# Optimization experiments

Measured on AMD Instinct MI355X. Metric: run time of the kernel, lower is better.

Reference implementation:

```python
import jax, jax.numpy as jnp
import numpy as np

B, T, H, V, L = 16, 256, 512, 32, 2


def setup_inputs() -> dict:
    key = jax.random.key(0)
    ks = jax.random.split(key, 24)
    s = 1.0 / np.sqrt(H)
    d = {}
    d["encoder_outputs"] = jax.random.normal(ks[0], (B, T, H), jnp.float32)
    d["h0"] = jax.random.normal(ks[1], (L, B, H), jnp.float32)
    d["c0"] = jax.random.normal(ks[2], (L, B, H), jnp.float32)
    d["audio_lengths"] = jax.random.randint(ks[3], (B,), 1, T + 1, jnp.int32)
    d["Wq"] = jax.random.normal(ks[4], (H, H), jnp.float32) * s
    d["bq"] = jnp.zeros((H,), jnp.float32)
    d["Wk"] = jax.random.normal(ks[5], (H, H), jnp.float32) * s
    d["bk"] = jnp.zeros((H,), jnp.float32)
    d["v"] = jax.random.normal(ks[6], (H,), jnp.float32) * s
    d["vb"] = jnp.zeros((1,), jnp.float32)
    d["Wih0"] = jax.random.normal(ks[7], (4 * H, 2 * H), jnp.float32) * s
    d["bih0"] = jnp.zeros((4 * H,), jnp.float32)
    d["Whh0"] = jax.random.normal(ks[8], (4 * H, H), jnp.float32) * s
    d["bhh0"] = jnp.zeros((4 * H,), jnp.float32)
    d["Wih1"] = jax.random.normal(ks[9], (4 * H, H), jnp.float32) * s
    d["bih1"] = jnp.zeros((4 * H,), jnp.float32)
    d["Whh1"] = jax.random.normal(ks[10], (4 * H, H), jnp.float32) * s
    d["bhh1"] = jnp.zeros((4 * H,), jnp.float32)
    d["Wout"] = jax.random.normal(ks[11], (V, H), jnp.float32) * s
    d["bout"] = jnp.zeros((V,), jnp.float32)
    return d


def _lstm_cell(x, h, c, Wih, bih, Whh, bhh):
    # PyTorch gate order: i, f, g, o
    g = x @ Wih.T + bih + h @ Whh.T + bhh
    i, f, gg, o = jnp.split(g, 4, axis=-1)
    c2 = jax.nn.sigmoid(f) * c + jax.nn.sigmoid(i) * jnp.tanh(gg)
    h2 = jax.nn.sigmoid(o) * jnp.tanh(c2)
    return h2, c2


def reference(encoder_outputs, h0, c0, audio_lengths, Wq, bq, Wk, bk, v, vb,
              Wih0, bih0, Whh0, bhh0, Wih1, bih1, Whh1, bhh1, Wout, bout):
    # Precompute key projection once (same math as per-step Wk @ keys)
    Kproj = encoder_outputs @ Wk.T + bk  # [B,T,H]

    def step(carry, enc_t):
        h, c = carry  # each [L,B,H]
        q = h[-1]  # [B,H] top-layer hidden drives attention
        e = jnp.tanh((q @ Wq.T + bq)[:, None, :] + Kproj)  # [B,T,H]
        scores = jnp.einsum('bth,h->bt', e, v) + vb[0]  # [B,T]
        w = jax.nn.softmax(scores, axis=-1)
        ctx = jnp.einsum('bt,bth->bh', w, encoder_outputs)  # [B,H]
        x = jnp.concatenate([enc_t, ctx], axis=-1)  # [B,2H]
        h0n, c0n = _lstm_cell(x, h[0], c[0], Wih0, bih0, Whh0, bhh0)
        h1n, c1n = _lstm_cell(h0n, h[1], c[1], Wih1, bih1, Whh1, bhh1)
        logit = h1n @ Wout.T + bout  # [B,V]
        return (jnp.stack([h0n, h1n]), jnp.stack([c0n, c1n])), logit

    _, logits = jax.lax.scan(step, (h0, c0), jnp.swapaxes(encoder_outputs, 0, 1))
    return jnp.swapaxes(logits, 0, 1)  # [B,T,V]
```

## Files before the change

kernel.cpp:

```cpp
#include <hip/hip_runtime.h>

#define HH 512
#define BB 16
#define TT 256
#define VV 32
#define TPB 256
#define NBLK 256
#define PITCH 516

#define BAR_INTS 512

struct KArgs {
  const float* enc; const float* h0in; const float* c0in;
  const float* Wq; const float* bq; const float* vatt; const float* vb;
  const float* Wih0; const float* bih0; const float* Whh0; const float* bhh0;
  const float* Wih1; const float* bih1; const float* Whh1; const float* bhh1;
  const float* Wout; const float* bout;
  const float* Kproj; float* H0buf; float* H1buf; float* qWg; float* Ug; float* Zg;
  int* bar; float* out;
};

struct Smem {
  float W0e[4][2][PITCH];
  float W0c[4][2][PITCH];
  float W0h[4][2][PITCH];
  float W1x[4][2][PITCH];
  float W1h[4][2][PITCH];
  float Wqr[2][PITCH];
  float Wor[2][PITCH];
  float vv[HH];
  float qrow[HH];
  float stg[BB][PITCH];
  float red[4][64];
  float pre0[BB][4][2];
  float pre1[BB][4][2];
  float cst[2][2][BB];
  float scw[16];
  float zinv[BB];
  float bs0[4][2];
  float bs1[4][2];
  float bqv[2], boutv[2];
};

__device__ __forceinline__ float fsig(float x){ return 1.0f/(1.0f + __expf(-x)); }
__device__ __forceinline__ float ftanh(float x){
  float ee = __expf(2.0f*x);
  return 1.0f - 2.0f/(ee + 1.0f);
}

__device__ __forceinline__ void stcc(float* p, float v){
  __hip_atomic_store(p, v, __ATOMIC_RELAXED, __HIP_MEMORY_SCOPE_AGENT);
}
__device__ __forceinline__ float ldcc(const float* p){
  return __hip_atomic_load(p, __ATOMIC_RELAXED, __HIP_MEMORY_SCOPE_AGENT);
}
__device__ __forceinline__ float2 ld2cc(const float* p){
  unsigned long long v = __hip_atomic_load((const unsigned long long*)p,
                                           __ATOMIC_RELAXED, __HIP_MEMORY_SCOPE_AGENT);
  union { unsigned long long u; float2 f; } c; c.u = v;
  return c.f;
}

__device__ __forceinline__ void ldbuf_cc(const float* __restrict__ src,
                                         float2* __restrict__ v, int tid){
  #pragma unroll
  for (int it = 0; it < 16; ++it)
    v[it] = ld2cc(&src[(it*TPB + tid)*2]);
}
__device__ __forceinline__ void stg_regs(const float2* __restrict__ v,
                                         float (* __restrict__ stg)[PITCH], int tid){
  #pragma unroll
  for (int it = 0; it < 16; ++it){
    const int i2 = (it*TPB + tid)*2;
    *(float2*)&stg[i2 >> 9][i2 & 511] = v[it];
  }
}

__device__ __forceinline__ void gbar_arrive(int* __restrict__ bar, int e, int bid){
  __syncthreads();
  if (threadIdx.x == 0)
    __hip_atomic_store(&bar[bid], e, __ATOMIC_RELAXED, __HIP_MEMORY_SCOPE_AGENT);
}
__device__ __forceinline__ void gbar_wait(int* __restrict__ bar, int e, int bid){
  if (threadIdx.x < 64){
    const unsigned long long* p = (const unsigned long long*)bar;
    const int i0 = threadIdx.x * 2;
    int spins = 0;
    for (;;){
      unsigned long long v0 = __hip_atomic_load(&p[i0],     __ATOMIC_RELAXED, __HIP_MEMORY_SCOPE_AGENT);
      unsigned long long v1 = __hip_atomic_load(&p[i0 + 1], __ATOMIC_RELAXED, __HIP_MEMORY_SCOPE_AGENT);
      const int a0 = (int)v0, a1 = (int)(v0 >> 32), a2 = (int)v1, a3 = (int)(v1 >> 32);
      const int ok = (a0 >= e) & (a1 >= e) & (a2 >= e) & (a3 >= e);
      if (__all(ok)) break;
      __builtin_amdgcn_s_sleep(2);
      if (++spins > (1 << 20)) break;
    }
  }
  __syncthreads();
}
__device__ __forceinline__ void gbar(int* __restrict__ bar, int e, int bid){
  gbar_arrive(bar, e, bid);
  gbar_wait(bar, e, bid);
}

__device__ __forceinline__ void gbar2(int* __restrict__ bar2, int et, int bid, int ba){
  __syncthreads();
  if (threadIdx.x == 0)
    __hip_atomic_store(&bar2[bid], et, __ATOMIC_RELAXED, __HIP_MEMORY_SCOPE_AGENT);
  if (threadIdx.x < 64){
    const unsigned long long* p = (const unsigned long long*)bar2 + ba*8;
    int spins = 0;
    for (;;){
      int ok = 1;
      if (threadIdx.x < 8){
        unsigned long long v = __hip_atomic_load(&p[threadIdx.x], __ATOMIC_RELAXED, __HIP_MEMORY_SCOPE_AGENT);
        ok = ((int)v >= et) & ((int)(v >> 32) >= et);
      }
      if (__all(ok)) break;
      __builtin_amdgcn_s_sleep(1);
      if (++spins > (1 << 20)) break;
    }
  }
  __syncthreads();
}

__device__ __forceinline__ void dot_part(const float* __restrict__ W,
                                         const float (* __restrict__ stg)[PITCH],
                                         float (* __restrict__ red)[64],
                                         int wave, int lane){
  const int jj = wave >> 1, off = (wave & 1) << 8;
  const int b = lane & 15, g = lane >> 4;
  const float* wrow = W + (size_t)(g*2 + jj)*PITCH + off;
  const float* xrow = &stg[b][off];
  float acc = 0.f;
  #pragma unroll 8
  for (int h = 0; h < 256; h += 4){
    const float4 w4 = *(const float4*)&wrow[h];
    const float4 x4 = *(const float4*)&xrow[h];
    acc = fmaf(w4.x,x4.x, fmaf(w4.y,x4.y, fmaf(w4.z,x4.z, fmaf(w4.w,x4.w, acc))));
  }
  red[wave][lane] = acc;
}

__global__ void init_kernel(const float* __restrict__ h0in, float* __restrict__ H0buf,
                            float* __restrict__ H1buf, float* __restrict__ Ug,
                            float* __restrict__ Zg, int* __restrict__ bar){
  const int i = blockIdx.x*blockDim.x + threadIdx.x;
  if (i < BB*HH){
    H0buf[i] = h0in[i];
    H1buf[i] = h0in[BB*HH + i];
  }
  if (i < 2*BB*HH) Ug[i] = 0.0f;
  if (i < 32) Zg[i] = 0.0f;
  if (i < BAR_INTS) bar[i] = 0;
}

__global__ __launch_bounds__(256, 1) void kproj_kernel(const float* __restrict__ enc,
                                                       const float* __restrict__ Wk,
                                                       const float* __restrict__ bk,
                                                       float* __restrict__ Kproj){
  __shared__ float er[BB][PITCH];
  const int bid = blockIdx.x, tid = threadIdx.x;
  const int wave = tid >> 6, lane = tid & 63;
  const int r = lane & 15, q = lane >> 4;
  const int row0 = bid*16;
  #pragma unroll
  for (int it = 0; it < 8; ++it){
    const int idx = (it*256 + tid)*4;
    const int rr = idx >> 9, h = idx & 511;
    *(float4*)&er[rr][h] = *(const float4*)&enc[(size_t)(row0+rr)*HH + h];
  }
  __syncthreads();
  float4 xr[32];
  #pragma unroll
  for (int i = 0; i < 32; ++i) xr[i] = *(const float4*)&er[r][q*128 + i*4];
  for (int k = 0; k < 128; ++k){
    const int hk = wave*128 + k;
    const float* wrow = Wk + (size_t)hk*HH + q*128;
    float acc = 0.f;
    #pragma unroll
    for (int i = 0; i < 32; ++i){
      const float4 w4 = *(const float4*)&wrow[i*4];
      acc = fmaf(w4.x,xr[i].x, fmaf(w4.y,xr[i].y, fmaf(w4.z,xr[i].z, fmaf(w4.w,xr[i].w, acc))));
    }
    acc += __shfl_xor(acc, 16);
    acc += __shfl_xor(acc, 32);
    if (lane < 16) Kproj[(size_t)(row0 + r)*HH + hk] = acc + bk[hk];
  }
}

__global__ __launch_bounds__(TPB, 1) void decoder_persist(KArgs a){
  __shared__ Smem S;
  const int bid = blockIdx.x, tid = threadIdx.x;
  const int wave = tid >> 6, lane = tid & 63;
  const int lb = lane & 15, lg = lane >> 4;
  const int j0 = bid*2;
  const int ba = bid >> 4, tb = (bid & 15) * 16;
  int* bar2 = a.bar + 256;

  for (int g = 0; g < 4; ++g){
    for (int jj = 0; jj < 2; ++jj){
      const int row = g*HH + j0 + jj;
      for (int h = tid; h < HH; h += TPB){
        S.W0e[g][jj][h] = a.Wih0[(size_t)row*(2*HH) + h];
        S.W0c[g][jj][h] = a.Wih0[(size_t)row*(2*HH) + HH + h];
        S.W0h[g][jj][h] = a.Whh0[(size_t)row*HH + h];
        S.W1x[g][jj][h] = a.Wih1[(size_t)row*HH + h];
        S.W1h[g][jj][h] = a.Whh1[(size_t)row*HH + h];
      }
    }
  }
  for (int jj = 0; jj < 2; ++jj){
    const int d = bid*2 + jj, vo = d & 31;
    for (int h = tid; h < HH; h += TPB){
      S.Wqr[jj][h] = a.Wq[(size_t)(j0+jj)*HH + h];
      S.Wor[jj][h] = a.Wout[(size_t)vo*HH + h];
    }
  }
  for (int h = tid; h < HH; h += TPB) S.vv[h] = a.vatt[h];
  if (tid < 16){
    S.cst[0][0][tid] = a.c0in[0*BB*HH + tid*HH + j0];
    S.cst[0][1][tid] = a.c0in[0*BB*HH + tid*HH + j0 + 1];
    S.cst[1][0][tid] = a.c0in[1*BB*HH + tid*HH + j0];
    S.cst[1][1][tid] = a.c0in[1*BB*HH + tid*HH + j0 + 1];
  }
  if (tid < 8){
    const int g = tid & 3, jj = tid >> 2;
    const int row = g*HH + j0 + jj;
    S.bs0[g][jj] = a.bih0[row] + a.bhh0[row];
    S.bs1[g][jj] = a.bih1[row] + a.bhh1[row];
  }
  if (tid < 2){
    S.bqv[tid] = a.bq[j0 + tid];
    S.boutv[tid] = a.bout[(bid*2 + tid) & 31];
  }
  const float vb0 = a.vb[0];

  float r_kp[4][8];
  #pragma unroll
  for (int i = 0; i < 4; ++i){
    const float* kp = a.Kproj + (size_t)(ba*TT + tb + wave*4 + i)*HH;
    #pragma unroll
    for (int k = 0; k < 8; ++k) r_kp[i][k] = kp[lane + 64*k];
  }
  float r_e0[16], r_e1[16];
  #pragma unroll
  for (int lt = 0; lt < 16; ++lt){
    const float* er = a.enc + (size_t)(ba*TT + tb + lt)*HH;
    r_e0[lt] = er[tid];
    r_e1[lt] = er[tid + 256];
  }
  float4 r_en[8];
  #pragma unroll
  for (int it = 0; it < 8; ++it){
    const int idx = (it*TPB + tid)*4;
    r_en[it] = *(const float4*)&a.enc[(size_t)((idx >> 9)*TT + 0)*HH + (idx & 511)];
  }
  __syncthreads();

  {
    #pragma unroll
    for (int it = 0; it < 8; ++it){
      const int idx = (it*TPB + tid)*4;
      *(float4*)&S.stg[idx >> 9][idx & 511] = *(const float4*)&a.h0in[idx];
    }
    __syncthreads();
    dot_part(&S.W0h[0][0][0], S.stg, S.red, wave, lane);
    __syncthreads();
    if (tid < 128){
      const int jj = tid >> 6, l = tid & 63, g = l >> 4, b = l & 15;
      S.pre0[b][g][jj] = S.red[2*jj][l] + S.red[2*jj+1][l] + S.bs0[g][jj];
    }
    __syncthreads();
  }

  int e = 0;
  for (int t = 0; t < TT; ++t){
    const int par = t & 1, parn = par ^ 1;

    float2 r_h1[16];
    ldbuf_cc(a.H1buf + par*(BB*HH), r_h1, tid);
    stg_regs(r_h1, S.stg, tid);
    __syncthreads();

    if (wave < 2){
      if (t > 0){
        const int d = bid*2 + wave, bo = d >> 5, vo = d & 31;
        float acc = 0.f;
        #pragma unroll
        for (int k = 0; k < 8; ++k){
          const int h = lane + 64*k;
          acc = fmaf(S.Wor[wave][h], S.stg[bo][h], acc);
        }
        #pragma unroll
        for (int off = 32; off; off >>= 1) acc += __shfl_xor(acc, off);
        if (lane == 0) a.out[(size_t)(bo*TT + (t-1))*VV + vo] = acc + S.boutv[wave];
      }
    } else {
      const int jj = wave - 2;
      const int off0 = lg * 128;
      float acc = 0.f;
      #pragma unroll 8
      for (int h = 0; h < 128; h += 4){
        const float4 w4 = *(const float4*)&S.Wqr[jj][off0 + h];
        const float4 x4 = *(const float4*)&S.stg[lb][off0 + h];
        acc = fmaf(w4.x,x4.x, fmaf(w4.y,x4.y, fmaf(w4.z,x4.z, fmaf(w4.w,x4.w, acc))));
      }
      acc += __shfl_xor(acc, 16);
      acc += __shfl_xor(acc, 32);
      if (lane < 16) stcc(&a.qWg[lane*HH + j0 + jj], acc + S.bqv[jj]);
    }

    e++; gbar_arrive(a.bar, e, bid);

    dot_part(&S.W1h[0][0][0], S.stg, S.red, wave, lane);
    __syncthreads();
    if (tid < 128){
      const int jj = tid >> 6, l = tid & 63, g = l >> 4, b = l & 15;
      S.pre1[b][g][jj] = S.red[2*jj][l] + S.red[2*jj+1][l] + S.bs1[g][jj];
    }
    #pragma unroll
    for (int it = 0; it < 8; ++it){
      const int idx = (it*TPB + tid)*4;
      *(float4*)&S.stg[idx >> 9][idx & 511] = r_en[it];
    }
    __syncthreads();
    dot_part(&S.W0e[0][0][0], S.stg, S.red, wave, lane);
    __syncthreads();
    if (tid < 128){
      const int jj = tid >> 6, l = tid & 63, g = l >> 4, b = l & 15;
      S.pre0[b][g][jj] += S.red[2*jj][l] + S.red[2*jj+1][l];
    }

    gbar_wait(a.bar, e, bid);

    {
      float* Up = a.Ug + par*(BB*HH);
      float* Zp = a.Zg + par*16;
      const float2 q2 = ld2cc(&a.qWg[ba*HH + tid*2]);
      *(float2*)&S.qrow[tid*2] = q2;
      __syncthreads();
      #pragma unroll
      for (int i = 0; i < 4; ++i){
        float acc = 0.f;
        #pragma unroll
        for (int k = 0; k < 8; ++k){
          const int h = lane + 64*k;
          acc = fmaf(S.vv[h], ftanh(S.qrow[h] + r_kp[i][k]), acc);
        }
        #pragma unroll
        for (int off = 32; off; off >>= 1) acc += __shfl_xor(acc, off);
        if (lane == 0) S.scw[wave*4 + i] = __expf(acc + vb0);
      }
      __syncthreads();
      float u0 = 0.f, u1 = 0.f;
      #pragma unroll
      for (int lt = 0; lt < 16; ++lt){
        const float w = S.scw[lt];
        u0 = fmaf(w, r_e0[lt], u0);
        u1 = fmaf(w, r_e1[lt], u1);
      }
      unsafeAtomicAdd(&Up[ba*HH + tid],       u0);
      unsafeAtomicAdd(&Up[ba*HH + tid + 256], u1);
      if (tid == 0){
        float zs = 0.f;
        #pragma unroll
        for (int lt = 0; lt < 16; ++lt) zs += S.scw[lt];
        unsafeAtomicAdd(&Zp[ba], zs);
      }
    }
    gbar2(bar2, t + 1, bid, ba);

    {
      float2 r_u[16];
      ldbuf_cc(a.Ug + par*(BB*HH), r_u, tid);
      if (tid < 16) S.zinv[tid] = 1.0f / ldcc(&a.Zg[par*16 + tid]);
      stg_regs(r_u, S.stg, tid);
      __syncthreads();
      dot_part(&S.W0c[0][0][0], S.stg, S.red, wave, lane);
      __syncthreads();
      if (tid < 32){
        const int b = tid & 15, jj = tid >> 4;
        const float zi = S.zinv[b];
        float gv[4];
        #pragma unroll
        for (int g = 0; g < 4; ++g)
          gv[g] = S.pre0[b][g][jj] + (S.red[2*jj][g*16+b] + S.red[2*jj+1][g*16+b]) * zi;
        const float cold = S.cst[0][jj][b];
        const float ii = fsig(gv[0]), ff = fsig(gv[1]);
        const float gg = ftanh(gv[2]), oo = fsig(gv[3]);
        const float cn = ff*cold + ii*gg;
        S.cst[0][jj][b] = cn;
        stcc(&a.H0buf[parn*(BB*HH) + b*HH + j0 + jj], oo * ftanh(cn));
      }
    }
    e++; gbar_arrive(a.bar, e, bid);
    {
      const int tn = (t + 1 < TT) ? (t + 1) : t;
      #pragma unroll
      for (int it = 0; it < 8; ++it){
        const int idx = (it*TPB + tid)*4;
        r_en[it] = *(const float4*)&a.enc[(size_t)((idx >> 9)*TT + tn)*HH + (idx & 511)];
      }
    }
    gbar_wait(a.bar, e, bid);

    {
      if (tid < 32) stcc(&a.Ug[parn*(BB*HH) + bid*32 + tid], 0.0f);
      if (bid == 0 && tid < 16) stcc(&a.Zg[parn*16 + tid], 0.0f);

      float2 r_x[16];
      ldbuf_cc(a.H0buf + parn*(BB*HH), r_x, tid);
      stg_regs(r_x, S.stg, tid);
      __syncthreads();
      dot_part(&S.W1x[0][0][0], S.stg, S.red, wave, lane);
      __syncthreads();
      if (tid < 32){
        const int b = tid & 15, jj = tid >> 4;
        float gv[4];
        #pragma unroll
        for (int g = 0; g < 4; ++g)
          gv[g] = S.pre1[b][g][jj] + S.red[2*jj][g*16+b] + S.red[2*jj+1][g*16+b];
        const float cold = S.cst[1][jj][b];
        const float ii = fsig(gv[0]), ff = fsig(gv[1]);
        const float gg = ftanh(gv[2]), oo = fsig(gv[3]);
        const float cn = ff*cold + ii*gg;
        S.cst[1][jj][b] = cn;
        stcc(&a.H1buf[parn*(BB*HH) + b*HH + j0 + jj], oo * ftanh(cn));
      }
    }
    e++; gbar_arrive(a.bar, e, bid);
    {
      dot_part(&S.W0h[0][0][0], S.stg, S.red, wave, lane);
      __syncthreads();
      if (tid < 128){
        const int jj = tid >> 6, l = tid & 63, g = l >> 4, b = l & 15;
        S.pre0[b][g][jj] = S.red[2*jj][l] + S.red[2*jj+1][l] + S.bs0[g][jj];
      }
    }
    gbar_wait(a.bar, e, bid);
  }

  {
    float2 r_x[16];
    ldbuf_cc(a.H1buf, r_x, tid);
    stg_regs(r_x, S.stg, tid);
    __syncthreads();
    if (wave < 2){
      const int d = bid*2 + wave, bo = d >> 5, vo = d & 31;
      float acc = 0.f;
      #pragma unroll
      for (int k = 0; k < 8; ++k){
        const int h = lane + 64*k;
        acc = fmaf(S.Wor[wave][h], S.stg[bo][h], acc);
      }
      #pragma unroll
      for (int off = 32; off; off >>= 1) acc += __shfl_xor(acc, off);
      if (lane == 0) a.out[(size_t)(bo*TT + 255)*VV + vo] = acc + S.boutv[wave];
    }
  }
}

extern "C" void kernel_launch(void* const* d_in, const int* in_sizes, int n_in,
                              void* d_out, int out_size, void* d_ws, size_t ws_size,
                              hipStream_t stream){
  const float* enc  = (const float*)d_in[0];
  const float* h0in = (const float*)d_in[1];
  const float* c0in = (const float*)d_in[2];
  const float* Wq   = (const float*)d_in[4];
  const float* bq   = (const float*)d_in[5];
  const float* Wk   = (const float*)d_in[6];
  const float* bk   = (const float*)d_in[7];
  const float* vatt = (const float*)d_in[8];
  const float* vb   = (const float*)d_in[9];
  const float* Wih0 = (const float*)d_in[10];
  const float* bih0 = (const float*)d_in[11];
  const float* Whh0 = (const float*)d_in[12];
  const float* bhh0 = (const float*)d_in[13];
  const float* Wih1 = (const float*)d_in[14];
  const float* bih1 = (const float*)d_in[15];
  const float* Whh1 = (const float*)d_in[16];
  const float* bhh1 = (const float*)d_in[17];
  const float* Wout = (const float*)d_in[18];
  const float* bout = (const float*)d_in[19];

  float* ws    = (float*)d_ws;
  float* Kproj = ws;
  float* H0buf = Kproj + (size_t)BB*TT*HH;
  float* H1buf = H0buf + 2*BB*HH;
  float* qWg   = H1buf + 2*BB*HH;
  float* Ug    = qWg + BB*HH;
  float* Zg    = Ug + 2*BB*HH;
  int*   bar   = (int*)(Zg + 32);

  hipLaunchKernelGGL(init_kernel, dim3(64), dim3(256), 0, stream,
                     h0in, H0buf, H1buf, Ug, Zg, bar);
  hipLaunchKernelGGL(kproj_kernel, dim3(256), dim3(256), 0, stream, enc, Wk, bk, Kproj);

  KArgs ka;
  ka.enc = enc; ka.h0in = h0in; ka.c0in = c0in;
  ka.Wq = Wq; ka.bq = bq; ka.vatt = vatt; ka.vb = vb;
  ka.Wih0 = Wih0; ka.bih0 = bih0; ka.Whh0 = Whh0; ka.bhh0 = bhh0;
  ka.Wih1 = Wih1; ka.bih1 = bih1; ka.Whh1 = Whh1; ka.bhh1 = bhh1;
  ka.Wout = Wout; ka.bout = bout;
  ka.Kproj = Kproj; ka.H0buf = H0buf; ka.H1buf = H1buf;
  ka.qWg = qWg; ka.Ug = Ug; ka.Zg = Zg; ka.bar = bar; ka.out = (float*)d_out;

  void* params[] = { (void*)&ka };
  hipLaunchCooperativeKernel((const void*)decoder_persist, dim3(NBLK), dim3(TPB),
                             params, 0, stream);
}
```

Measured before the change: 5.321 ms.

## Double threads per block to 512 and split dot products across eight waves

Raises the persistent kernel's block size from 256 to 512 threads, so every per-step gate matvec is split over eight waves with a four-way partial reduction instead of two-way. Per-thread register arrays, the attention key-projection tiles and the encoder context accumulation are halved to match. The reduction scratch is unioned with the query row to save LDS, and the inner loops use multiple accumulators for more ILP. Each latency-bound recurrent step is meant to finish sooner, at the cost of more intra-block synchronisation and a larger final reduction.

```diff
diff --git a/kernel.cpp b/kernel.cpp
--- a/kernel.cpp
+++ b/kernel.cpp
@@ -4,7 +4,7 @@
 #define BB 16
 #define TT 256
 #define VV 32
-#define TPB 256
+#define TPB 512
 #define NBLK 256
 #define PITCH 516
 
@@ -29,9 +29,8 @@
   float Wqr[2][PITCH];
   float Wor[2][PITCH];
   float vv[HH];
-  float qrow[HH];
+  union { float qrow[HH]; float red[8][64]; } qr;
   float stg[BB][PITCH];
-  float red[4][64];
   float pre0[BB][4][2];
   float pre1[BB][4][2];
   float cst[2][2][BB];
@@ -64,13 +63,13 @@
 __device__ __forceinline__ void ldbuf_cc(const float* __restrict__ src,
                                          float2* __restrict__ v, int tid){
   #pragma unroll
-  for (int it = 0; it < 16; ++it)
+  for (int it = 0; it < 8; ++it)
     v[it] = ld2cc(&src[(it*TPB + tid)*2]);
 }
 __device__ __forceinline__ void stg_regs(const float2* __restrict__ v,
                                          float (* __restrict__ stg)[PITCH], int tid){
   #pragma unroll
-  for (int it = 0; it < 16; ++it){
+  for (int it = 0; it < 8; ++it){
     const int i2 = (it*TPB + tid)*2;
     *(float2*)&stg[i2 >> 9][i2 & 511] = v[it];
   }
@@ -98,10 +97,6 @@
   }
   __syncthreads();
 }
-__device__ __forceinline__ void gbar(int* __restrict__ bar, int e, int bid){
-  gbar_arrive(bar, e, bid);
-  gbar_wait(bar, e, bid);
-}
 
 __device__ __forceinline__ void gbar2(int* __restrict__ bar2, int et, int bid, int ba){
   __syncthreads();
@@ -124,22 +119,27 @@
   __syncthreads();
 }
 
-__device__ __forceinline__ void dot_part(const float* __restrict__ W,
-                                         const float (* __restrict__ stg)[PITCH],
-                                         float (* __restrict__ red)[64],
-                                         int wave, int lane){
-  const int jj = wave >> 1, off = (wave & 1) << 8;
+__device__ __forceinline__ void dot8(const float* __restrict__ W,
+                                     const float (* __restrict__ stg)[PITCH],
+                                     float (* __restrict__ red)[64],
+                                     int wave, int lane){
+  const int jj = wave >> 2, off = (wave & 3) << 7;
   const int b = lane & 15, g = lane >> 4;
   const float* wrow = W + (size_t)(g*2 + jj)*PITCH + off;
   const float* xrow = &stg[b][off];
-  float acc = 0.f;
-  #pragma unroll 8
-  for (int h = 0; h < 256; h += 4){
-    const float4 w4 = *(const float4*)&wrow[h];
-    const float4 x4 = *(const float4*)&xrow[h];
-    acc = fmaf(w4.x,x4.x, fmaf(w4.y,x4.y, fmaf(w4.z,x4.z, fmaf(w4.w,x4.w, acc))));
-  }
-  red[wave][lane] = acc;
+  float a0 = 0.f, a1 = 0.f, a2 = 0.f, a3 = 0.f;
+  #pragma unroll
+  for (int h = 0; h < 128; h += 16){
+    const float4 w0 = *(const float4*)&wrow[h];      const float4 x0 = *(const float4*)&xrow[h];
+    const float4 w1 = *(const float4*)&wrow[h + 4];  const float4 x1 = *(const float4*)&xrow[h + 4];
+    const float4 w2 = *(const float4*)&wrow[h + 8];  const float4 x2 = *(const float4*)&xrow[h + 8];
+    const float4 w3 = *(const float4*)&wrow[h + 12]; const float4 x3 = *(const float4*)&xrow[h + 12];
+    a0 = fmaf(w0.x,x0.x, fmaf(w0.y,x0.y, fmaf(w0.z,x0.z, fmaf(w0.w,x0.w, a0))));
+    a1 = fmaf(w1.x,x1.x, fmaf(w1.y,x1.y, fmaf(w1.z,x1.z, fmaf(w1.w,x1.w, a1))));
+    a2 = fmaf(w2.x,x2.x, fmaf(w2.y,x2.y, fmaf(w2.z,x2.z, fmaf(w2.w,x2.w, a2))));
+    a3 = fmaf(w3.x,x3.x, fmaf(w3.y,x3.y, fmaf(w3.z,x3.z, fmaf(w3.w,x3.w, a3))));
+  }
+  red[wave][lane] = (a0 + a1) + (a2 + a3);
 }
 
 __global__ void init_kernel(const float* __restrict__ h0in, float* __restrict__ H0buf,
@@ -236,23 +236,20 @@
   }
   const float vb0 = a.vb[0];
 
-  float r_kp[4][8];
-  #pragma unroll
-  for (int i = 0; i < 4; ++i){
-    const float* kp = a.Kproj + (size_t)(ba*TT + tb + wave*4 + i)*HH;
+  float r_kp[2][8];
+  #pragma unroll
+  for (int i = 0; i < 2; ++i){
+    const float* kp = a.Kproj + (size_t)(ba*TT + tb + wave*2 + i)*HH;
     #pragma unroll
     for (int k = 0; k < 8; ++k) r_kp[i][k] = kp[lane + 64*k];
   }
-  float r_e0[16], r_e1[16];
-  #pragma unroll
-  for (int lt = 0; lt < 16; ++lt){
-    const float* er = a.enc + (size_t)(ba*TT + tb + lt)*HH;
-    r_e0[lt] = er[tid];
-    r_e1[lt] = er[tid + 256];
-  }
-  float4 r_en[8];
-  #pragma unroll
-  for (int it = 0; it < 8; ++it){
+  float r_e[16];
+  #pragma unroll
+  for (int lt = 0; lt < 16; ++lt)
+    r_e[lt] = a.enc[(size_t)(ba*TT + tb + lt)*HH + tid];
+  float4 r_en[4];
+  #pragma unroll
+  for (int it = 0; it < 4; ++it){
     const int idx = (it*TPB + tid)*4;
     r_en[it] = *(const float4*)&a.enc[(size_t)((idx >> 9)*TT + 0)*HH + (idx & 511)];
   }
@@ -260,16 +257,17 @@
 
   {
     #pragma unroll
-    for (int it = 0; it < 8; ++it){
+    for (int it = 0; it < 4; ++it){
       const int idx = (it*TPB + tid)*4;
       *(float4*)&S.stg[idx >> 9][idx & 511] = *(const float4*)&a.h0in[idx];
     }
     __syncthreads();
-    dot_part(&S.W0h[0][0][0], S.stg, S.red, wave, lane);
+    dot8(&S.W0h[0][0][0], S.stg, S.qr.red, wave, lane);
     __syncthreads();
     if (tid < 128){
       const int jj = tid >> 6, l = tid & 63, g = l >> 4, b = l & 15;
-      S.pre0[b][g][jj] = S.red[2*jj][l] + S.red[2*jj+1][l] + S.bs0[g][jj];
+      S.pre0[b][g][jj] = (S.qr.red[jj*4+0][l] + S.qr.red[jj*4+1][l])
+                       + (S.qr.red[jj*4+2][l] + S.qr.red[jj*4+3][l]) + S.bs0[g][jj];
     }
     __syncthreads();
   }
@@ -278,7 +276,7 @@
   for (int t = 0; t < TT; ++t){
     const int par = t & 1, parn = par ^ 1;
 
-    float2 r_h1[16];
+    float2 r_h1[8];
     ldbuf_cc(a.H1buf + par*(BB*HH), r_h1, tid);
     stg_regs(r_h1, S.stg, tid);
     __syncthreads();
@@ -296,16 +294,20 @@
         for (int off = 32; off; off >>= 1) acc += __shfl_xor(acc, off);
         if (lane == 0) a.out[(size_t)(bo*TT + (t-1))*VV + vo] = acc + S.boutv[wave];
       }
-    } else {
+    } else if (wave < 4){
       const int jj = wave - 2;
       const int off0 = lg * 128;
-      float acc = 0.f;
-      #pragma unroll 8
-      for (int h = 0; h < 128; h += 4){
-        const float4 w4 = *(const float4*)&S.Wqr[jj][off0 + h];
-        const float4 x4 = *(const float4*)&S.stg[lb][off0 + h];
-        acc = fmaf(w4.x,x4.x, fmaf(w4.y,x4.y, fmaf(w4.z,x4.z, fmaf(w4.w,x4.w, acc))));
-      }
+      float a0 = 0.f, a1 = 0.f;
+      #pragma unroll
+      for (int h = 0; h < 128; h += 8){
+        const float4 w0 = *(const float4*)&S.Wqr[jj][off0 + h];
+        const float4 x0 = *(const float4*)&S.stg[lb][off0 + h];
+        const float4 w1 = *(const float4*)&S.Wqr[jj][off0 + h + 4];
+        const float4 x1 = *(const float4*)&S.stg[lb][off0 + h + 4];
+        a0 = fmaf(w0.x,x0.x, fmaf(w0.y,x0.y, fmaf(w0.z,x0.z, fmaf(w0.w,x0.w, a0))));
+        a1 = fmaf(w1.x,x1.x, fmaf(w1.y,x1.y, fmaf(w1.z,x1.z, fmaf(w1.w,x1.w, a1))));
+      }
+      float acc = a0 + a1;
       acc += __shfl_xor(acc, 16);
       acc += __shfl_xor(acc, 32);
       if (lane < 16) stcc(&a.qWg[lane*HH + j0 + jj], acc + S.bqv[jj]);
@@ -313,23 +315,25 @@
 
     e++; gbar_arrive(a.bar, e, bid);
 
-    dot_part(&S.W1h[0][0][0], S.stg, S.red, wave, lane);
+    dot8(&S.W1h[0][0][0], S.stg, S.qr.red, wave, lane);
     __syncthreads();
     if (tid < 128){
       const int jj = tid >> 6, l = tid & 63, g = l >> 4, b = l & 15;
-      S.pre1[b][g][jj] = S.red[2*jj][l] + S.red[2*jj+1][l] + S.bs1[g][jj];
+      S.pre1[b][g][jj] = (S.qr.red[jj*4+0][l] + S.qr.red[jj*4+1][l])
+                       + (S.qr.red[jj*4+2][l] + S.qr.red[jj*4+3][l]) + S.bs1[g][jj];
     }
     #pragma unroll
-    for (int it = 0; it < 8; ++it){
+    for (int it = 0; it < 4; ++it){
       const int idx = (it*TPB + tid)*4;
       *(float4*)&S.stg[idx >> 9][idx & 511] = r_en[it];
     }
     __syncthreads();
-    dot_part(&S.W0e[0][0][0], S.stg, S.red, wave, lane);
+    dot8(&S.W0e[0][0][0], S.stg, S.qr.red, wave, lane);
     __syncthreads();
     if (tid < 128){
       const int jj = tid >> 6, l = tid & 63, g = l >> 4, b = l & 15;
-      S.pre0[b][g][jj] += S.red[2*jj][l] + S.red[2*jj+1][l];
+      S.pre0[b][g][jj] += (S.qr.red[jj*4+0][l] + S.qr.red[jj*4+1][l])
+                        + (S.qr.red[jj*4+2][l] + S.qr.red[jj*4+3][l]);
     }
 
     gbar_wait(a.bar, e, bid);
@@ -337,31 +341,27 @@
     {
       float* Up = a.Ug + par*(BB*HH);
       float* Zp = a.Zg + par*16;
-      const float2 q2 = ld2cc(&a.qWg[ba*HH + tid*2]);
-      *(float2*)&S.qrow[tid*2] = q2;
+      const float qv = ldcc(&a.qWg[ba*HH + tid]);
+      S.qr.qrow[tid] = qv;
       __syncthreads();
       #pragma unroll
-      for (int i = 0; i < 4; ++i){
+      for (int i = 0; i < 2; ++i){
         float acc = 0.f;
         #pragma unroll
         for (int k = 0; k < 8; ++k){
           const int h = lane + 64*k;
-          acc = fmaf(S.vv[h], ftanh(S.qrow[h] + r_kp[i][k]), acc);
+          acc = fmaf(S.vv[h], ftanh(S.qr.qrow[h] + r_kp[i][k]), acc);
         }
         #pragma unroll
         for (int off = 32; off; off >>= 1) acc += __shfl_xor(acc, off);
-        if (lane == 0) S.scw[wave*4 + i] = __expf(acc + vb0);
-      }
-      __syncthreads();
-      float u0 = 0.f, u1 = 0.f;
+        if (lane == 0) S.scw[wave*2 + i] = __expf(acc + vb0);
+      }
+      __syncthreads();
+      float u = 0.f;
       #pragma unroll
-      for (int lt = 0; lt < 16; ++lt){
-        const float w = S.scw[lt];
-        u0 = fmaf(w, r_e0[lt], u0);
-        u1 = fmaf(w, r_e1[lt], u1);
-      }
-      unsafeAtomicAdd(&Up[ba*HH + tid],       u0);
-      unsafeAtomicAdd(&Up[ba*HH + tid + 256], u1);
+      for (int lt = 0; lt < 16; ++lt)
+        u = fmaf(S.scw[lt], r_e[lt], u);
+      unsafeAtomicAdd(&Up[ba*HH + tid], u);
       if (tid == 0){
         float zs = 0.f;
         #pragma unroll
@@ -372,20 +372,24 @@
     gbar2(bar2, t + 1, bid, ba);
 
     {
-      float2 r_u[16];
+      float2 r_u[8];
       ldbuf_cc(a.Ug + par*(BB*HH), r_u, tid);
       if (tid < 16) S.zinv[tid] = 1.0f / ldcc(&a.Zg[par*16 + tid]);
       stg_regs(r_u, S.stg, tid);
       __syncthreads();
-      dot_part(&S.W0c[0][0][0], S.stg, S.red, wave, lane);
+      dot8(&S.W0c[0][0][0], S.stg, S.qr.red, wave, lane);
       __syncthreads();
       if (tid < 32){
         const int b = tid & 15, jj = tid >> 4;
         const float zi = S.zinv[b];
         float gv[4];
         #pragma unroll
-        for (int g = 0; g < 4; ++g)
-          gv[g] = S.pre0[b][g][jj] + (S.red[2*jj][g*16+b] + S.red[2*jj+1][g*16+b]) * zi;
+        for (int g = 0; g < 4; ++g){
+          const int l = g*16 + b;
+          gv[g] = S.pre0[b][g][jj]
+                + ((S.qr.red[jj*4+0][l] + S.qr.red[jj*4+1][l])
+                 + (S.qr.red[jj*4+2][l] + S.qr.red[jj*4+3][l])) * zi;
+        }
         const float cold = S.cst[0][jj][b];
         const float ii = fsig(gv[0]), ff = fsig(gv[1]);
         const float gg = ftanh(gv[2]), oo = fsig(gv[3]);
@@ -398,7 +402,7 @@
     {
       const int tn = (t + 1 < TT) ? (t + 1) : t;
       #pragma unroll
-      for (int it = 0; it < 8; ++it){
+      for (int it = 0; it < 4; ++it){
         const int idx = (it*TPB + tid)*4;
         r_en[it] = *(const float4*)&a.enc[(size_t)((idx >> 9)*TT + tn)*HH + (idx & 511)];
       }
@@ -409,18 +413,22 @@
       if (tid < 32) stcc(&a.Ug[parn*(BB*HH) + bid*32 + tid], 0.0f);
       if (bid == 0 && tid < 16) stcc(&a.Zg[parn*16 + tid], 0.0f);
 
-      float2 r_x[16];
+      float2 r_x[8];
       ldbuf_cc(a.H0buf + parn*(BB*HH), r_x, tid);
       stg_regs(r_x, S.stg, tid);
       __syncthreads();
-      dot_part(&S.W1x[0][0][0], S.stg, S.red, wave, lane);
+      dot8(&S.W1x[0][0][0], S.stg, S.qr.red, wave, lane);
       __syncthreads();
       if (tid < 32){
         const int b = tid & 15, jj = tid >> 4;
         float gv[4];
         #pragma unroll
-        for (int g = 0; g < 4; ++g)
-          gv[g] = S.pre1[b][g][jj] + S.red[2*jj][g*16+b] + S.red[2*jj+1][g*16+b];
+        for (int g = 0; g < 4; ++g){
+          const int l = g*16 + b;
+          gv[g] = S.pre1[b][g][jj]
+                + (S.qr.red[jj*4+0][l] + S.qr.red[jj*4+1][l])
+                + (S.qr.red[jj*4+2][l] + S.qr.red[jj*4+3][l]);
+        }
         const float cold = S.cst[1][jj][b];
         const float ii = fsig(gv[0]), ff = fsig(gv[1]);
         const float gg = ftanh(gv[2]), oo = fsig(gv[3]);
@@ -431,18 +439,19 @@
     }
     e++; gbar_arrive(a.bar, e, bid);
     {
-      dot_part(&S.W0h[0][0][0], S.stg, S.red, wave, lane);
+      dot8(&S.W0h[0][0][0], S.stg, S.qr.red, wave, lane);
       __syncthreads();
       if (tid < 128){
         const int jj = tid >> 6, l = tid & 63, g = l >> 4, b = l & 15;
-        S.pre0[b][g][jj] = S.red[2*jj][l] + S.red[2*jj+1][l] + S.bs0[g][jj];
+        S.pre0[b][g][jj] = (S.qr.red[jj*4+0][l] + S.qr.red[jj*4+1][l])
+                         + (S.qr.red[jj*4+2][l] + S.qr.red[jj*4+3][l]) + S.bs0[g][jj];
       }
     }
     gbar_wait(a.bar, e, bid);
   }
 
   {
-    float2 r_x[16];
+    float2 r_x[8];
     ldbuf_cc(a.H1buf, r_x, tid);
     stg_regs(r_x, S.stg, tid);
     __syncthreads();
```

After: 4.705 ms (median of 2 runs). 11.6% less time.
